# Kernel tuning notes

Measured on AMD Instinct MI355X. Metric: run time of the kernel, lower is better.

## Reference

```python
import jax, jax.numpy as jnp
import numpy as np

RENORM_PERIOD = 256
MAX_NORM = 100.0


def setup_inputs() -> dict:
    key = jax.random.key(0)
    ks = jax.random.split(key, 9)
    B, S, G, D, N = 4, 2048, 8, 128, 64
    return {
        "x_r": jax.random.normal(ks[0], (B, S, G, D), jnp.float32),
        "x_i": jax.random.normal(ks[1], (B, S, G, D), jnp.float32),
        "log_A_mag": jax.random.uniform(ks[2], (G, N), jnp.float32) * 0.5 + 0.5,
        "A_phase": jax.random.normal(ks[3], (G, N), jnp.float32) * 0.1,
        "Bw_r": jax.random.normal(ks[4], (N, D), jnp.float32) / np.sqrt(D),
        "Bw_i": jax.random.normal(ks[5], (N, D), jnp.float32) / np.sqrt(D),
        "Cw_r": jax.random.normal(ks[6], (D, N), jnp.float32) / np.sqrt(N),
        "Cw_i": jax.random.normal(ks[7], (D, N), jnp.float32) / np.sqrt(N),
        "dt_w": jax.random.normal(ks[8], (2, 2 * D), jnp.float32) * 0.02,
        "dt_b": jnp.zeros((2,), jnp.float32),
    }


def reference(x_r, x_i, log_A_mag, A_phase, Bw_r, Bw_i, Cw_r, Cw_i, dt_w, dt_b):
    B, S, G, D = x_r.shape
    N = Bw_r.shape[0]
    # dt: input-dependent step magnitude / phase scale, clamped
    x_cat = jnp.concatenate([x_r, x_i], axis=-1)            # [B,S,G,2D]
    dt = jnp.clip(jnp.exp(jnp.einsum('bsgd,od->bsgo', x_cat, dt_w) + dt_b), 1e-4, 2.0)
    dt_mag = dt[..., 0:1]                                    # [B,S,G,1]
    dt_phase = dt[..., 1:2]
    # A_bar in polar form, |A| = exp(-softplus(log_A_mag)*dt_mag) < 1
    neg_log_A = -jax.nn.softplus(log_A_mag)[None, None]      # [1,1,G,N]
    A_mag = jnp.exp(dt_mag * neg_log_A)                      # [B,S,G,N]
    A_ang = dt_phase * A_phase[None, None]
    A_r = A_mag * jnp.cos(A_ang)
    A_i = A_mag * jnp.sin(A_ang)
    # Bx = (B_proj @ x) * dt_mag, complex linear
    Bx_r = (jnp.einsum('bsgd,nd->bsgn', x_r, Bw_r) - jnp.einsum('bsgd,nd->bsgn', x_i, Bw_i)) * dt_mag
    Bx_i = (jnp.einsum('bsgd,nd->bsgn', x_r, Bw_i) + jnp.einsum('bsgd,nd->bsgn', x_i, Bw_r)) * dt_mag

    def step(carry, inp):
        h_r, h_i = carry
        ar, ai, br, bi, t = inp
        nh_r = ar * h_r - ai * h_i + br
        nh_i = ar * h_i + ai * h_r + bi
        renorm = ((t + 1) % RENORM_PERIOD) == 0
        norm = jnp.sqrt(nh_r * nh_r + nh_i * nh_i + 1e-8)
        scale = jnp.minimum(norm, MAX_NORM) / norm
        nh_r = jnp.where(renorm, nh_r * scale, nh_r)
        nh_i = jnp.where(renorm, nh_i * scale, nh_i)
        return (nh_r, nh_i), (nh_r, nh_i)

    h0 = (jnp.zeros((B, G, N), jnp.float32), jnp.zeros((B, G, N), jnp.float32))
    xs = (jnp.moveaxis(A_r, 1, 0), jnp.moveaxis(A_i, 1, 0),
          jnp.moveaxis(Bx_r, 1, 0), jnp.moveaxis(Bx_i, 1, 0),
          jnp.arange(S))
    _, (all_h_r, all_h_i) = jax.lax.scan(step, h0, xs)       # [S,B,G,N]
    all_h_r = jnp.moveaxis(all_h_r, 0, 1)                    # [B,S,G,N]
    all_h_i = jnp.moveaxis(all_h_i, 0, 1)
    # y = C_proj(h), complex linear N -> D
    y_r = jnp.einsum('bsgn,dn->bsgd', all_h_r, Cw_r) - jnp.einsum('bsgn,dn->bsgd', all_h_i, Cw_i)
    y_i = jnp.einsum('bsgn,dn->bsgd', all_h_r, Cw_i) + jnp.einsum('bsgn,dn->bsgd', all_h_i, Cw_r)
    return jnp.stack([y_r, y_i], axis=0)                     # [2,B,S,G,D]
```

## Files before the change

### kernel.cpp

```cpp
#include <hip/hip_runtime.h>
#include <math.h>

#define B_ 4
#define S_ 2048
#define G_ 8
#define D_ 128
#define N_ 64
#define ROWS (B_*S_*G_)
#define CH 64
#define CLEN 32
#define NCHAIN (B_*G_*N_)
#define YOFF (ROWS*D_)

typedef short bf16x8 __attribute__((ext_vector_type(8)));
typedef float f32x4  __attribute__((ext_vector_type(4)));
#define MFMA16(a,b,c) __builtin_amdgcn_mfma_f32_16x16x32_bf16(a,b,c,0,0,0)

__device__ __forceinline__ unsigned short bf16_rtne(float f) {
    unsigned u = __float_as_uint(f);
    unsigned r = (u + 0x7FFFu + ((u >> 16) & 1u)) >> 16;
    return (unsigned short)r;
}
__device__ __forceinline__ void split_bf16(float f, unsigned short &hi, unsigned short &lo) {
    hi = bf16_rtne(f);
    float hif = __uint_as_float(((unsigned)hi) << 16);
    lo = bf16_rtne(f - hif);
}
__device__ __forceinline__ void split4(float4 v, uint2 &hi2, uint2 &lo2) {
    unsigned short h0,h1,h2,h3,l0,l1,l2,l3;
    split_bf16(v.x,h0,l0); split_bf16(v.y,h1,l1);
    split_bf16(v.z,h2,l2); split_bf16(v.w,h3,l3);
    hi2 = make_uint2((unsigned)h0 | ((unsigned)h1<<16), (unsigned)h2 | ((unsigned)h3<<16));
    lo2 = make_uint2((unsigned)l0 | ((unsigned)l1<<16), (unsigned)l2 | ((unsigned)l3<<16));
}
__device__ __forceinline__ float dot4(float4 a, float4 b) {
    return fmaf(a.x,b.x, fmaf(a.y,b.y, fmaf(a.z,b.z, a.w*b.w)));
}

__global__ __launch_bounds__(256) void k_prep(
    const float* __restrict__ bwr, const float* __restrict__ bwi,
    const float* __restrict__ cwr, const float* __restrict__ cwi,
    unsigned short* __restrict__ wbhi, unsigned short* __restrict__ wblo,
    unsigned short* __restrict__ wchi)
{
    int tid = blockIdx.x * 256 + threadIdx.x;
    if (tid < 4096) {
        int f = tid;
        int lane = f & 63, ks = (f >> 6) & 7, nt = (f >> 9) & 1, w = f >> 10;
        int l15 = lane & 15, quad = lane >> 4;
        int n = w * 32 + nt * 16 + l15;
        int k0 = ks * 32 + quad * 8;
        const float* src; float sgn = 1.f;
        if (n < 64) {
            if (k0 < 128) src = bwr + n * 128 + k0;
            else        { src = bwi + n * 128 + (k0 - 128); sgn = -1.f; }
        } else {
            if (k0 < 128) src = bwi + (n - 64) * 128 + k0;
            else          src = bwr + (n - 64) * 128 + (k0 - 128);
        }
        float4 v0 = *(const float4*)src;
        float4 v1 = *(const float4*)(src + 4);
        float vv[8] = {v0.x,v0.y,v0.z,v0.w,v1.x,v1.y,v1.z,v1.w};
        unsigned short h[8], l[8];
        #pragma unroll
        for (int j = 0; j < 8; j++) split_bf16(vv[j] * sgn, h[j], l[j]);
        #pragma unroll
        for (int j = 0; j < 8; j++) { wbhi[f*8+j] = h[j]; wblo[f*8+j] = l[j]; }
    } else {
        int f = tid - 4096;
        int lane = f & 63, ks = (f >> 6) & 3, nt = (f >> 8) & 3, w = f >> 10;
        int l15 = lane & 15, quad = lane >> 4;
        int n = w * 64 + nt * 16 + l15;
        int d = (n < 128) ? n : (n - 128);
        int k0 = ks * 32 + quad * 8;
        const float* src; float sgn = 1.f;
        if (n < 128) {
            if (k0 < 64) src = cwr + d * 64 + k0;
            else       { src = cwi + d * 64 + (k0 - 64); sgn = -1.f; }
        } else {
            if (k0 < 64) src = cwi + d * 64 + k0;
            else         src = cwr + d * 64 + (k0 - 64);
        }
        float4 v0 = *(const float4*)src;
        float4 v1 = *(const float4*)(src + 4);
        float vv[8] = {v0.x,v0.y,v0.z,v0.w,v1.x,v1.y,v1.z,v1.w};
        unsigned short h[8], l[8];
        #pragma unroll
        for (int j = 0; j < 8; j++) split_bf16(vv[j] * sgn, h[j], l[j]);
        #pragma unroll
        for (int j = 0; j < 8; j++) wchi[f*8+j] = h[j];
    }
}

#define LDK1 280
__global__ __launch_bounds__(256, 2) void k_g1(
    const float* __restrict__ xr, const float* __restrict__ xi,
    const float* __restrict__ dtw, const float* __restrict__ dtb,
    const float* __restrict__ logAm, const float* __restrict__ Aph,
    const unsigned short* __restrict__ wbhi, const unsigned short* __restrict__ wblo,
    float* __restrict__ bxr, float* __restrict__ bxi,
    float* __restrict__ dt_mag, float* __restrict__ dt_ph,
    float4* __restrict__ trans)
{
    __shared__ __align__(16) unsigned short Ahi[32 * LDK1];
    __shared__ __align__(16) unsigned short Alo[32 * LDK1];
    __shared__ float dms[32], dps[32];
    __shared__ float4 comb[64];
    float* bxs = (float*)Ahi;
    const int t = threadIdx.x;
    const int lane = t & 63, w = t >> 6;
    const int l15 = lane & 15, quad = lane >> 4;
    const int bg = blockIdx.x >> 4, cq = blockIdx.x & 15;
    const int g = bg & 7, b = bg >> 3;

    bf16x8 wh[2][8], wl[2][8];
    #pragma unroll
    for (int nt = 0; nt < 2; nt++)
        #pragma unroll
        for (int ks = 0; ks < 8; ks++) {
            int idx = ((w * 2 + nt) * 8 + ks) * 64 + lane;
            wh[nt][ks] = ((const bf16x8*)wbhi)[idx];
            wl[nt][ks] = ((const bf16x8*)wblo)[idx];
        }

    const int kq = t & 31, k4 = kq * 4;
    float4 w0r = *(const float4*)(dtw + k4);
    float4 w0i = *(const float4*)(dtw + 128 + k4);
    float4 w1r = *(const float4*)(dtw + 256 + k4);
    float4 w1i = *(const float4*)(dtw + 384 + k4);
    float b0 = dtb[0], b1 = dtb[1];
    float nla = -logf(1.0f + __expf(logAm[g * N_ + lane]));
    float aph = Aph[g * N_ + lane];

    for (int it = 0; it < 4; it++) {
        __syncthreads();
        const int c  = cq * 4 + it;
        const int s0 = c * CLEN;
        const float* xrb = xr + ((size_t)(b * S_ + s0) * G_ + g) * 128;
        const float* xib = xi + ((size_t)(b * S_ + s0) * G_ + g) * 128;
        float pm[4], pp[4];
        #pragma unroll
        for (int i = 0; i < 4; i++) {
            int f = t + 256 * i;
            int m = f >> 5, kk = f & 31;
            float4 a  = ((const float4*)(xrb + m * 1024))[kk];
            float4 bb = ((const float4*)(xib + m * 1024))[kk];
            uint2 h2, l2;
            split4(a, h2, l2);
            *(uint2*)&Ahi[m * LDK1 + kk * 4] = h2;
            *(uint2*)&Alo[m * LDK1 + kk * 4] = l2;
            split4(bb, h2, l2);
            *(uint2*)&Ahi[m * LDK1 + 128 + kk * 4] = h2;
            *(uint2*)&Alo[m * LDK1 + 128 + kk * 4] = l2;
            pm[i] = dot4(a, w0r) + dot4(bb, w0i);
            pp[i] = dot4(a, w1r) + dot4(bb, w1i);
        }
        #pragma unroll
        for (int i = 0; i < 4; i++) {
            float vm = pm[i], vp = pp[i];
            #pragma unroll
            for (int msk = 16; msk >= 1; msk >>= 1) {
                vm += __shfl_xor(vm, msk);
                vp += __shfl_xor(vp, msk);
            }
            if ((t & 31) == 0) {
                int m = (t >> 5) + 8 * i;
                float dm = fminf(fmaxf(__expf(vm + b0), 1e-4f), 2.0f);
                float dp = fminf(fmaxf(__expf(vp + b1), 1e-4f), 2.0f);
                dms[m] = dm; dps[m] = dp;
                int row = (b * S_ + s0 + m) * G_ + g;
                dt_mag[row] = dm; dt_ph[row] = dp;
            }
        }
        __syncthreads();

        f32x4 acc[2][2];
        #pragma unroll
        for (int a = 0; a < 2; a++)
            #pragma unroll
            for (int bq = 0; bq < 2; bq++)
                acc[a][bq] = (f32x4){0.f, 0.f, 0.f, 0.f};
        #pragma unroll
        for (int ms = 0; ms < 2; ms++) {
            int arow = (ms * 16 + l15) * LDK1 + quad * 8;
            #pragma unroll
            for (int ks = 0; ks < 8; ks++) {
                bf16x8 ah = *(const bf16x8*)&Ahi[arow + ks * 32];
                bf16x8 al = *(const bf16x8*)&Alo[arow + ks * 32];
                #pragma unroll
                for (int nt = 0; nt < 2; nt++) {
                    acc[ms][nt] = MFMA16(al, wh[nt][ks], acc[ms][nt]);
                    acc[ms][nt] = MFMA16(ah, wl[nt][ks], acc[ms][nt]);
                    acc[ms][nt] = MFMA16(ah, wh[nt][ks], acc[ms][nt]);
                }
            }
        }
        __syncthreads();

        #pragma unroll
        for (int ms = 0; ms < 2; ms++)
            #pragma unroll
            for (int nt = 0; nt < 2; nt++) {
                int n = w * 32 + nt * 16 + l15;
                float* dstg = (n < 64) ? bxr : bxi;
                int nn = n & 63;
                #pragma unroll
                for (int r = 0; r < 4; r++) {
                    int m = ms * 16 + quad * 4 + r;
                    float v = acc[ms][nt][r] * dms[m];
                    dstg[((b * S_ + s0 + m) * G_ + g) * 64 + nn] = v;
                    bxs[m * 132 + n] = v;
                }
            }
        __syncthreads();

        float Ar = 1.f, Ai = 0.f, Br = 0.f, Bi = 0.f;
        if (w < 2) {
            int base = w * 16;
            #pragma unroll
            for (int tt = 0; tt < 16; tt++) {
                int m = base + tt;
                float dm = dms[m], dp = dps[m];
                float am  = __expf(dm * nla);
                float ang = dp * aph;
                float cr = am * __cosf(ang), ci = am * __sinf(ang);
                float vr = bxs[m * 132 + lane], vi = bxs[m * 132 + 64 + lane];
                float nAr = cr * Ar - ci * Ai;
                float nAi = cr * Ai + ci * Ar;
                float nBr = cr * Br - ci * Bi + vr;
                float nBi = cr * Bi + ci * Br + vi;
                Ar = nAr; Ai = nAi; Br = nBr; Bi = nBi;
            }
            if (w == 0) comb[lane] = make_float4(Ar, Ai, Br, Bi);
        }
        __syncthreads();
        if (w == 1) {
            float4 c0 = comb[lane];
            float fAr = Ar * c0.x - Ai * c0.y;
            float fAi = Ar * c0.y + Ai * c0.x;
            float fBr = Ar * c0.z - Ai * c0.w + Br;
            float fBi = Ar * c0.w + Ai * c0.z + Bi;
            trans[(bg * CH + c) * 64 + lane] = make_float4(fAr, fAi, fBr, fBi);
        }
    }
}

__global__ __launch_bounds__(256) void k_scanB2(const float4* __restrict__ trans,
    float2* __restrict__ hstart)
{
    int w = threadIdx.x >> 6, lane = threadIdx.x & 63;
    int W = blockIdx.x * 4 + w;
    int bg = W >> 3;
    int n  = ((W & 7) << 3) + (lane & 7);
    int j  = lane >> 3;
    float pAr[8], pAi[8], pBr[8], pBi[8];
    float Ar = 1.f, Ai = 0.f, Br = 0.f, Bi = 0.f;
    const float4* tp = trans + (bg * CH + j * 8) * 64 + n;
    #pragma unroll
    for (int k = 0; k < 8; k++) {
        pAr[k] = Ar; pAi[k] = Ai; pBr[k] = Br; pBi[k] = Bi;
        float4 T = tp[k * 64];
        float nAr = T.x * Ar - T.y * Ai;
        float nAi = T.x * Ai + T.y * Ar;
        float nBr = T.x * Br - T.y * Bi + T.z;
        float nBi = T.x * Bi + T.y * Br + T.w;
        Ar = nAr; Ai = nAi; Br = nBr; Bi = nBi;
    }
    float hr = 0.f, hi = 0.f, mhr = 0.f, mhi = 0.f;
    #pragma unroll
    for (int j2 = 0; j2 < 8; j2++) {
        if (j2 == j) { mhr = hr; mhi = hi; }
        int src = j2 * 8 + (lane & 7);
        float sAr = __shfl(Ar, src), sAi = __shfl(Ai, src);
        float sBr = __shfl(Br, src), sBi = __shfl(Bi, src);
        float nr = sAr * hr - sAi * hi + sBr;
        float ni = sAr * hi + sAi * hr + sBi;
        float nrm = sqrtf(nr * nr + ni * ni + 1e-8f);
        float sc = fminf(nrm, 100.f) / nrm;
        hr = nr * sc; hi = ni * sc;
    }
    float2* hp = hstart + (bg * CH + j * 8) * 64 + n;
    #pragma unroll
    for (int k = 0; k < 8; k++) {
        float hsr = pAr[k] * mhr - pAi[k] * mhi + pBr[k];
        float hsi = pAr[k] * mhi + pAi[k] * mhr + pBi[k];
        hp[k * 64] = make_float2(hsr, hsi);
    }
}

#define LDK2 152
__global__ __launch_bounds__(256, 2) void k_sg2(
    const float* __restrict__ bxr, const float* __restrict__ bxi,
    const float* __restrict__ dt_mag, const float* __restrict__ dt_ph,
    const float* __restrict__ logAm, const float* __restrict__ Aph,
    const float2* __restrict__ hstart,
    const unsigned short* __restrict__ wchi,
    float* __restrict__ out)
{
    __shared__ __align__(16) unsigned short Ahi[128 * LDK2];
    __shared__ __align__(16) unsigned short Alo[128 * LDK2];
    const int t = threadIdx.x;
    const int lane = t & 63, w = t >> 6;
    const int l15 = lane & 15, quad = lane >> 4;
    const int bg = blockIdx.x >> 4, cq = blockIdx.x & 15;
    const int g = bg & 7, b = bg >> 3;

    bf16x8 wc[4][4];
    #pragma unroll
    for (int nt = 0; nt < 4; nt++)
        #pragma unroll
        for (int ks = 0; ks < 4; ks++)
            wc[nt][ks] = ((const bf16x8*)wchi)[((w * 4 + nt) * 4 + ks) * 64 + lane];

    {
        const int n = lane;
        const int c = cq * 4 + w;
        float nla = -logf(1.0f + __expf(logAm[g * N_ + n]));
        float aph = Aph[g * N_ + n];
        float2 h0 = hstart[(bg * CH + c) * 64 + n];
        float hr = h0.x, hi = h0.y;
        const bool rn = ((c & 7) == 7);
        const int rowbase = (b * S_ + c * CLEN) * G_ + g;
        #pragma unroll 8
        for (int tt = 0; tt < CLEN; tt++) {
            int row = rowbase + tt * G_;
            float dm = dt_mag[row], dp = dt_ph[row];
            float am  = __expf(dm * nla);
            float ang = dp * aph;
            float cr = am * __cosf(ang), ci = am * __sinf(ang);
            float vr = bxr[row * N_ + n], vi = bxi[row * N_ + n];
            float nr = cr * hr - ci * hi + vr;
            float ni = cr * hi + ci * hr + vi;
            if (rn && tt == CLEN - 1) {
                float nrm = sqrtf(nr * nr + ni * ni + 1e-8f);
                float scale = fminf(nrm, 100.0f) / nrm;
                nr *= scale; ni *= scale;
            }
            hr = nr; hi = ni;
            int m = w * 32 + tt;
            unsigned short hh, hl;
            split_bf16(hr, hh, hl);
            Ahi[m * LDK2 + n] = hh;  Alo[m * LDK2 + n] = hl;
            split_bf16(hi, hh, hl);
            Ahi[m * LDK2 + 64 + n] = hh;  Alo[m * LDK2 + 64 + n] = hl;
        }
    }
    __syncthreads();

    #pragma unroll
    for (int mh = 0; mh < 2; mh++) {
        f32x4 acc[4][4];
        #pragma unroll
        for (int a = 0; a < 4; a++)
            #pragma unroll
            for (int bq = 0; bq < 4; bq++)
                acc[a][bq] = (f32x4){0.f, 0.f, 0.f, 0.f};
        #pragma unroll
        for (int ms = 0; ms < 4; ms++) {
            int arow = (mh * 64 + ms * 16 + l15) * LDK2 + quad * 8;
            #pragma unroll
            for (int ks = 0; ks < 4; ks++) {
                bf16x8 ah = *(const bf16x8*)&Ahi[arow + ks * 32];
                bf16x8 al = *(const bf16x8*)&Alo[arow + ks * 32];
                #pragma unroll
                for (int nt = 0; nt < 4; nt++) {
                    acc[ms][nt] = MFMA16(al, wc[nt][ks], acc[ms][nt]);
                    acc[ms][nt] = MFMA16(ah, wc[nt][ks], acc[ms][nt]);
                }
            }
        }
        #pragma unroll
        for (int ms = 0; ms < 4; ms++)
            #pragma unroll
            for (int nt = 0; nt < 4; nt++) {
                int nn = w * 64 + nt * 16 + l15;
                float* dst = (nn < 128) ? (out + nn) : (out + YOFF + (nn - 128));
                #pragma unroll
                for (int r = 0; r < 4; r++) {
                    int m_local = mh * 64 + ms * 16 + quad * 4 + r;
                    int cc = m_local >> 5, tt2 = m_local & 31;
                    int srow = (b * S_ + (cq * 4 + cc) * CLEN + tt2) * G_ + g;
                    dst[srow * 128] = acc[ms][nt][r];
                }
            }
    }
}

extern "C" void kernel_launch(void* const* d_in, const int* in_sizes, int n_in,
                              void* d_out, int out_size, void* d_ws, size_t ws_size,
                              hipStream_t stream) {
    (void)in_sizes; (void)n_in; (void)out_size; (void)ws_size;
    const float* xr    = (const float*)d_in[0];
    const float* xi    = (const float*)d_in[1];
    const float* logAm = (const float*)d_in[2];
    const float* Aph   = (const float*)d_in[3];
    const float* bwr   = (const float*)d_in[4];
    const float* bwi   = (const float*)d_in[5];
    const float* cwr   = (const float*)d_in[6];
    const float* cwi   = (const float*)d_in[7];
    const float* dtw   = (const float*)d_in[8];
    const float* dtb   = (const float*)d_in[9];
    float* out = (float*)d_out;
    float* ws  = (float*)d_ws;

    float*  dt_mag = ws;
    float*  dt_ph  = ws + 65536;
    float*  bxr    = ws + 131072;
    float*  bxi    = bxr + 4194304;
    float4* trans  = (float4*)(ws + 8519680);
    float2* hstart = (float2*)(ws + 9043968);
    unsigned short* wbhi = (unsigned short*)(ws + 9306112);
    unsigned short* wblo = wbhi + 32768;
    unsigned short* wchi = wblo + 32768;

    hipLaunchKernelGGL(k_prep,   dim3(32), dim3(256), 0, stream,
                       bwr, bwi, cwr, cwi, wbhi, wblo, wchi);
    hipLaunchKernelGGL(k_g1,     dim3((B_ * G_) * 16), dim3(256), 0, stream,
                       xr, xi, dtw, dtb, logAm, Aph, wbhi, wblo,
                       bxr, bxi, dt_mag, dt_ph, trans);
    hipLaunchKernelGGL(k_scanB2, dim3(64), dim3(256), 0, stream,
                       trans, hstart);
    hipLaunchKernelGGL(k_sg2,    dim3((B_ * G_) * 16), dim3(256), 0, stream,
                       bxr, bxi, dt_mag, dt_ph, logAm, Aph, hstart, wchi, out);
}
```

Baseline: 161.6 us.

## Split chunk loops across more blocks and stream weights per k-step

k_g1 now launches one block per 32-step chunk instead of looping over four chunks per block, and k_sg2 handles two chunks per block instead of four, with its shared tile halved. Both kernels drop the register-resident weight fragments and reload them from global memory (L2-resident) inside the k loop, and their launch bounds rise to four blocks per CU. The intent is to fill the GPU with more blocks and more resident waves to hide latency. The cost is repeated weight loads and per-block setup for every chunk, and in k_sg2 half the waves sit idle during the scan phase.

```diff
diff --git a/kernel.cpp b/kernel.cpp
--- a/kernel.cpp
+++ b/kernel.cpp
@@ -93,7 +93,7 @@
 }
 
 #define LDK1 280
-__global__ __launch_bounds__(256, 2) void k_g1(
+__global__ __launch_bounds__(256, 4) void k_g1(
     const float* __restrict__ xr, const float* __restrict__ xi,
     const float* __restrict__ dtw, const float* __restrict__ dtb,
     const float* __restrict__ logAm, const float* __restrict__ Aph,
@@ -110,18 +110,8 @@
     const int t = threadIdx.x;
     const int lane = t & 63, w = t >> 6;
     const int l15 = lane & 15, quad = lane >> 4;
-    const int bg = blockIdx.x >> 4, cq = blockIdx.x & 15;
+    const int bg = blockIdx.x >> 6, c = blockIdx.x & 63;
     const int g = bg & 7, b = bg >> 3;
-
-    bf16x8 wh[2][8], wl[2][8];
-    #pragma unroll
-    for (int nt = 0; nt < 2; nt++)
-        #pragma unroll
-        for (int ks = 0; ks < 8; ks++) {
-            int idx = ((w * 2 + nt) * 8 + ks) * 64 + lane;
-            wh[nt][ks] = ((const bf16x8*)wbhi)[idx];
-            wl[nt][ks] = ((const bf16x8*)wblo)[idx];
-        }
 
     const int kq = t & 31, k4 = kq * 4;
     float4 w0r = *(const float4*)(dtw + k4);
@@ -132,116 +122,117 @@
     float nla = -logf(1.0f + __expf(logAm[g * N_ + lane]));
     float aph = Aph[g * N_ + lane];
 
-    for (int it = 0; it < 4; it++) {
-        __syncthreads();
-        const int c  = cq * 4 + it;
-        const int s0 = c * CLEN;
-        const float* xrb = xr + ((size_t)(b * S_ + s0) * G_ + g) * 128;
-        const float* xib = xi + ((size_t)(b * S_ + s0) * G_ + g) * 128;
-        float pm[4], pp[4];
-        #pragma unroll
-        for (int i = 0; i < 4; i++) {
-            int f = t + 256 * i;
-            int m = f >> 5, kk = f & 31;
-            float4 a  = ((const float4*)(xrb + m * 1024))[kk];
-            float4 bb = ((const float4*)(xib + m * 1024))[kk];
-            uint2 h2, l2;
-            split4(a, h2, l2);
-            *(uint2*)&Ahi[m * LDK1 + kk * 4] = h2;
-            *(uint2*)&Alo[m * LDK1 + kk * 4] = l2;
-            split4(bb, h2, l2);
-            *(uint2*)&Ahi[m * LDK1 + 128 + kk * 4] = h2;
-            *(uint2*)&Alo[m * LDK1 + 128 + kk * 4] = l2;
-            pm[i] = dot4(a, w0r) + dot4(bb, w0i);
-            pp[i] = dot4(a, w1r) + dot4(bb, w1i);
-        }
-        #pragma unroll
-        for (int i = 0; i < 4; i++) {
-            float vm = pm[i], vp = pp[i];
-            #pragma unroll
-            for (int msk = 16; msk >= 1; msk >>= 1) {
-                vm += __shfl_xor(vm, msk);
-                vp += __shfl_xor(vp, msk);
-            }
-            if ((t & 31) == 0) {
-                int m = (t >> 5) + 8 * i;
-                float dm = fminf(fmaxf(__expf(vm + b0), 1e-4f), 2.0f);
-                float dp = fminf(fmaxf(__expf(vp + b1), 1e-4f), 2.0f);
-                dms[m] = dm; dps[m] = dp;
-                int row = (b * S_ + s0 + m) * G_ + g;
-                dt_mag[row] = dm; dt_ph[row] = dp;
-            }
-        }
-        __syncthreads();
-
-        f32x4 acc[2][2];
-        #pragma unroll
-        for (int a = 0; a < 2; a++)
-            #pragma unroll
-            for (int bq = 0; bq < 2; bq++)
-                acc[a][bq] = (f32x4){0.f, 0.f, 0.f, 0.f};
+    const int s0 = c * CLEN;
+    const float* xrb = xr + ((size_t)(b * S_ + s0) * G_ + g) * 128;
+    const float* xib = xi + ((size_t)(b * S_ + s0) * G_ + g) * 128;
+
+    float pm[4], pp[4];
+    #pragma unroll
+    for (int i = 0; i < 4; i++) {
+        int f = t + 256 * i;
+        int m = f >> 5, kk = f & 31;
+        float4 a  = ((const float4*)(xrb + m * 1024))[kk];
+        float4 bb = ((const float4*)(xib + m * 1024))[kk];
+        uint2 h2, l2;
+        split4(a, h2, l2);
+        *(uint2*)&Ahi[m * LDK1 + kk * 4] = h2;
+        *(uint2*)&Alo[m * LDK1 + kk * 4] = l2;
+        split4(bb, h2, l2);
+        *(uint2*)&Ahi[m * LDK1 + 128 + kk * 4] = h2;
+        *(uint2*)&Alo[m * LDK1 + 128 + kk * 4] = l2;
+        pm[i] = dot4(a, w0r) + dot4(bb, w0i);
+        pp[i] = dot4(a, w1r) + dot4(bb, w1i);
+    }
+    #pragma unroll
+    for (int i = 0; i < 4; i++) {
+        float vm = pm[i], vp = pp[i];
+        #pragma unroll
+        for (int msk = 16; msk >= 1; msk >>= 1) {
+            vm += __shfl_xor(vm, msk);
+            vp += __shfl_xor(vp, msk);
+        }
+        if ((t & 31) == 0) {
+            int m = (t >> 5) + 8 * i;
+            float dm = fminf(fmaxf(__expf(vm + b0), 1e-4f), 2.0f);
+            float dp = fminf(fmaxf(__expf(vp + b1), 1e-4f), 2.0f);
+            dms[m] = dm; dps[m] = dp;
+            int row = (b * S_ + s0 + m) * G_ + g;
+            dt_mag[row] = dm; dt_ph[row] = dp;
+        }
+    }
+    __syncthreads();
+
+    f32x4 acc[2][2];
+    #pragma unroll
+    for (int a = 0; a < 2; a++)
+        #pragma unroll
+        for (int bq = 0; bq < 2; bq++)
+            acc[a][bq] = (f32x4){0.f, 0.f, 0.f, 0.f};
+    #pragma unroll
+    for (int ks = 0; ks < 8; ks++) {
+        bf16x8 wh0 = ((const bf16x8*)wbhi)[((w * 2 + 0) * 8 + ks) * 64 + lane];
+        bf16x8 wl0 = ((const bf16x8*)wblo)[((w * 2 + 0) * 8 + ks) * 64 + lane];
+        bf16x8 wh1 = ((const bf16x8*)wbhi)[((w * 2 + 1) * 8 + ks) * 64 + lane];
+        bf16x8 wl1 = ((const bf16x8*)wblo)[((w * 2 + 1) * 8 + ks) * 64 + lane];
         #pragma unroll
         for (int ms = 0; ms < 2; ms++) {
             int arow = (ms * 16 + l15) * LDK1 + quad * 8;
+            bf16x8 ah = *(const bf16x8*)&Ahi[arow + ks * 32];
+            bf16x8 al = *(const bf16x8*)&Alo[arow + ks * 32];
+            acc[ms][0] = MFMA16(al, wh0, acc[ms][0]);
+            acc[ms][0] = MFMA16(ah, wl0, acc[ms][0]);
+            acc[ms][0] = MFMA16(ah, wh0, acc[ms][0]);
+            acc[ms][1] = MFMA16(al, wh1, acc[ms][1]);
+            acc[ms][1] = MFMA16(ah, wl1, acc[ms][1]);
+            acc[ms][1] = MFMA16(ah, wh1, acc[ms][1]);
+        }
+    }
+    __syncthreads();
+
+    #pragma unroll
+    for (int ms = 0; ms < 2; ms++)
+        #pragma unroll
+        for (int nt = 0; nt < 2; nt++) {
+            int n = w * 32 + nt * 16 + l15;
+            float* dstg = (n < 64) ? bxr : bxi;
+            int nn = n & 63;
             #pragma unroll
-            for (int ks = 0; ks < 8; ks++) {
-                bf16x8 ah = *(const bf16x8*)&Ahi[arow + ks * 32];
-                bf16x8 al = *(const bf16x8*)&Alo[arow + ks * 32];
-                #pragma unroll
-                for (int nt = 0; nt < 2; nt++) {
-                    acc[ms][nt] = MFMA16(al, wh[nt][ks], acc[ms][nt]);
-                    acc[ms][nt] = MFMA16(ah, wl[nt][ks], acc[ms][nt]);
-                    acc[ms][nt] = MFMA16(ah, wh[nt][ks], acc[ms][nt]);
-                }
+            for (int r = 0; r < 4; r++) {
+                int m = ms * 16 + quad * 4 + r;
+                float v = acc[ms][nt][r] * dms[m];
+                dstg[((b * S_ + s0 + m) * G_ + g) * 64 + nn] = v;
+                bxs[m * 132 + n] = v;
             }
         }
-        __syncthreads();
-
-        #pragma unroll
-        for (int ms = 0; ms < 2; ms++)
-            #pragma unroll
-            for (int nt = 0; nt < 2; nt++) {
-                int n = w * 32 + nt * 16 + l15;
-                float* dstg = (n < 64) ? bxr : bxi;
-                int nn = n & 63;
-                #pragma unroll
-                for (int r = 0; r < 4; r++) {
-                    int m = ms * 16 + quad * 4 + r;
-                    float v = acc[ms][nt][r] * dms[m];
-                    dstg[((b * S_ + s0 + m) * G_ + g) * 64 + nn] = v;
-                    bxs[m * 132 + n] = v;
-                }
-            }
-        __syncthreads();
-
-        float Ar = 1.f, Ai = 0.f, Br = 0.f, Bi = 0.f;
-        if (w < 2) {
-            int base = w * 16;
-            #pragma unroll
-            for (int tt = 0; tt < 16; tt++) {
-                int m = base + tt;
-                float dm = dms[m], dp = dps[m];
-                float am  = __expf(dm * nla);
-                float ang = dp * aph;
-                float cr = am * __cosf(ang), ci = am * __sinf(ang);
-                float vr = bxs[m * 132 + lane], vi = bxs[m * 132 + 64 + lane];
-                float nAr = cr * Ar - ci * Ai;
-                float nAi = cr * Ai + ci * Ar;
-                float nBr = cr * Br - ci * Bi + vr;
-                float nBi = cr * Bi + ci * Br + vi;
-                Ar = nAr; Ai = nAi; Br = nBr; Bi = nBi;
-            }
-            if (w == 0) comb[lane] = make_float4(Ar, Ai, Br, Bi);
-        }
-        __syncthreads();
-        if (w == 1) {
-            float4 c0 = comb[lane];
-            float fAr = Ar * c0.x - Ai * c0.y;
-            float fAi = Ar * c0.y + Ai * c0.x;
-            float fBr = Ar * c0.z - Ai * c0.w + Br;
-            float fBi = Ar * c0.w + Ai * c0.z + Bi;
-            trans[(bg * CH + c) * 64 + lane] = make_float4(fAr, fAi, fBr, fBi);
-        }
+    __syncthreads();
+
+    float Ar = 1.f, Ai = 0.f, Br = 0.f, Bi = 0.f;
+    if (w < 2) {
+        int base = w * 16;
+        #pragma unroll
+        for (int tt = 0; tt < 16; tt++) {
+            int m = base + tt;
+            float dm = dms[m], dp = dps[m];
+            float am  = __expf(dm * nla);
+            float ang = dp * aph;
+            float cr = am * __cosf(ang), ci = am * __sinf(ang);
+            float vr = bxs[m * 132 + lane], vi = bxs[m * 132 + 64 + lane];
+            float nAr = cr * Ar - ci * Ai;
+            float nAi = cr * Ai + ci * Ar;
+            float nBr = cr * Br - ci * Bi + vr;
+            float nBi = cr * Bi + ci * Br + vi;
+            Ar = nAr; Ai = nAi; Br = nBr; Bi = nBi;
+        }
+        if (w == 0) comb[lane] = make_float4(Ar, Ai, Br, Bi);
+    }
+    __syncthreads();
+    if (w == 1) {
+        float4 c0 = comb[lane];
+        float fAr = Ar * c0.x - Ai * c0.y;
+        float fAi = Ar * c0.y + Ai * c0.x;
+        float fBr = Ar * c0.z - Ai * c0.w + Br;
+        float fBi = Ar * c0.w + Ai * c0.z + Bi;
+        trans[(bg * CH + c) * 64 + lane] = make_float4(fAr, fAi, fBr, fBi);
     }
 }
 
@@ -289,7 +280,7 @@
 }
 
 #define LDK2 152
-__global__ __launch_bounds__(256, 2) void k_sg2(
+__global__ __launch_bounds__(256, 4) void k_sg2(
     const float* __restrict__ bxr, const float* __restrict__ bxi,
     const float* __restrict__ dt_mag, const float* __restrict__ dt_ph,
     const float* __restrict__ logAm, const float* __restrict__ Aph,
@@ -297,24 +288,17 @@
     const unsigned short* __restrict__ wchi,
     float* __restrict__ out)
 {
-    __shared__ __align__(16) unsigned short Ahi[128 * LDK2];
-    __shared__ __align__(16) unsigned short Alo[128 * LDK2];
+    __shared__ __align__(16) unsigned short Ahi[64 * LDK2];
+    __shared__ __align__(16) unsigned short Alo[64 * LDK2];
     const int t = threadIdx.x;
     const int lane = t & 63, w = t >> 6;
     const int l15 = lane & 15, quad = lane >> 4;
-    const int bg = blockIdx.x >> 4, cq = blockIdx.x & 15;
+    const int bg = blockIdx.x >> 5, cp = blockIdx.x & 31;
     const int g = bg & 7, b = bg >> 3;
 
-    bf16x8 wc[4][4];
-    #pragma unroll
-    for (int nt = 0; nt < 4; nt++)
-        #pragma unroll
-        for (int ks = 0; ks < 4; ks++)
-            wc[nt][ks] = ((const bf16x8*)wchi)[((w * 4 + nt) * 4 + ks) * 64 + lane];
-
-    {
+    if (w < 2) {
         const int n = lane;
-        const int c = cq * 4 + w;
+        const int c = cp * 2 + w;
         float nla = -logf(1.0f + __expf(logAm[g * N_ + n]));
         float aph = Aph[g * N_ + n];
         float2 h0 = hstart[(bg * CH + c) * 64 + n];
@@ -347,43 +331,47 @@
     }
     __syncthreads();
 
-    #pragma unroll
-    for (int mh = 0; mh < 2; mh++) {
-        f32x4 acc[4][4];
-        #pragma unroll
-        for (int a = 0; a < 4; a++)
+    f32x4 acc[4][4];
+    #pragma unroll
+    for (int a = 0; a < 4; a++)
+        #pragma unroll
+        for (int bq = 0; bq < 4; bq++)
+            acc[a][bq] = (f32x4){0.f, 0.f, 0.f, 0.f};
+    #pragma unroll
+    for (int ks = 0; ks < 4; ks++) {
+        bf16x8 wc0 = ((const bf16x8*)wchi)[((w * 4 + 0) * 4 + ks) * 64 + lane];
+        bf16x8 wc1 = ((const bf16x8*)wchi)[((w * 4 + 1) * 4 + ks) * 64 + lane];
+        bf16x8 wc2 = ((const bf16x8*)wchi)[((w * 4 + 2) * 4 + ks) * 64 + lane];
+        bf16x8 wc3 = ((const bf16x8*)wchi)[((w * 4 + 3) * 4 + ks) * 64 + lane];
+        #pragma unroll
+        for (int ms = 0; ms < 4; ms++) {
+            int arow = (ms * 16 + l15) * LDK2 + quad * 8;
+            bf16x8 ah = *(const bf16x8*)&Ahi[arow + ks * 32];
+            bf16x8 al = *(const bf16x8*)&Alo[arow + ks * 32];
+            acc[ms][0] = MFMA16(al, wc0, acc[ms][0]);
+            acc[ms][0] = MFMA16(ah, wc0, acc[ms][0]);
+            acc[ms][1] = MFMA16(al, wc1, acc[ms][1]);
+            acc[ms][1] = MFMA16(ah, wc1, acc[ms][1]);
+            acc[ms][2] = MFMA16(al, wc2, acc[ms][2]);
+            acc[ms][2] = MFMA16(ah, wc2, acc[ms][2]);
+            acc[ms][3] = MFMA16(al, wc3, acc[ms][3]);
+            acc[ms][3] = MFMA16(ah, wc3, acc[ms][3]);
+        }
+    }
+    #pragma unroll
+    for (int ms = 0; ms < 4; ms++)
+        #pragma unroll
+        for (int nt = 0; nt < 4; nt++) {
+            int nn = w * 64 + nt * 16 + l15;
+            float* dst = (nn < 128) ? (out + nn) : (out + YOFF + (nn - 128));
             #pragma unroll
-            for (int bq = 0; bq < 4; bq++)
-                acc[a][bq] = (f32x4){0.f, 0.f, 0.f, 0.f};
-        #pragma unroll
-        for (int ms = 0; ms < 4; ms++) {
-            int arow = (mh * 64 + ms * 16 + l15) * LDK2 + quad * 8;
-            #pragma unroll
-            for (int ks = 0; ks < 4; ks++) {
-                bf16x8 ah = *(const bf16x8*)&Ahi[arow + ks * 32];
-                bf16x8 al = *(const bf16x8*)&Alo[arow + ks * 32];
-                #pragma unroll
-                for (int nt = 0; nt < 4; nt++) {
-                    acc[ms][nt] = MFMA16(al, wc[nt][ks], acc[ms][nt]);
-                    acc[ms][nt] = MFMA16(ah, wc[nt][ks], acc[ms][nt]);
-                }
+            for (int r = 0; r < 4; r++) {
+                int m_local = ms * 16 + quad * 4 + r;
+                int cc = m_local >> 5, tt2 = m_local & 31;
+                int srow = (b * S_ + (cp * 2 + cc) * CLEN + tt2) * G_ + g;
+                dst[srow * 128] = acc[ms][nt][r];
             }
         }
-        #pragma unroll
-        for (int ms = 0; ms < 4; ms++)
-            #pragma unroll
-            for (int nt = 0; nt < 4; nt++) {
-                int nn = w * 64 + nt * 16 + l15;
-                float* dst = (nn < 128) ? (out + nn) : (out + YOFF + (nn - 128));
-                #pragma unroll
-                for (int r = 0; r < 4; r++) {
-                    int m_local = mh * 64 + ms * 16 + quad * 4 + r;
-                    int cc = m_local >> 5, tt2 = m_local & 31;
-                    int srow = (b * S_ + (cq * 4 + cc) * CLEN + tt2) * G_ + g;
-                    dst[srow * 128] = acc[ms][nt][r];
-                }
-            }
-    }
 }
 
 extern "C" void kernel_launch(void* const* d_in, const int* in_sizes, int n_in,
@@ -415,11 +403,11 @@
 
     hipLaunchKernelGGL(k_prep,   dim3(32), dim3(256), 0, stream,
                        bwr, bwi, cwr, cwi, wbhi, wblo, wchi);
-    hipLaunchKernelGGL(k_g1,     dim3((B_ * G_) * 16), dim3(256), 0, stream,
+    hipLaunchKernelGGL(k_g1,     dim3((B_ * G_) * 64), dim3(256), 0, stream,
                        xr, xi, dtw, dtb, logAm, Aph, wbhi, wblo,
                        bxr, bxi, dt_mag, dt_ph, trans);
     hipLaunchKernelGGL(k_scanB2, dim3(64), dim3(256), 0, stream,
                        trans, hstart);
-    hipLaunchKernelGGL(k_sg2,    dim3((B_ * G_) * 16), dim3(256), 0, stream,
+    hipLaunchKernelGGL(k_sg2,    dim3((B_ * G_) * 32), dim3(256), 0, stream,
                        bxr, bxi, dt_mag, dt_ph, logAm, Aph, hstart, wchi, out);
 }
```

Result: no change. 160.3 us (-0.7%).
